# Kernel optimization log

Hardware: AMD Instinct MI355X
Metric: run time of the kernel (lower is better)

## Reference

```python
import jax, jax.numpy as jnp
import numpy as np

N_NODES = 200000
N_EDGES = 600000
IN_DIM = 130   # hidden_dim + 2
HID = 128
BN_EPS = 1e-5


def setup_inputs() -> dict:
    key = jax.random.key(0)
    ks = jax.random.split(key, 12)
    s = 0.05
    inp = {
        'x': jax.random.normal(ks[0], (N_NODES, IN_DIM), dtype=jnp.float32),
        'edge_index': jax.random.randint(ks[1], (2, N_EDGES), 0, N_NODES, dtype=jnp.int32),
        # SAGEConv 1: lin_l (aggregated neighbors, with bias), lin_r (root, no bias)
        'W1_l': jax.random.normal(ks[2], (IN_DIM, HID), dtype=jnp.float32) * s,
        'b1_l': jnp.zeros((HID,), dtype=jnp.float32),
        'W1_r': jax.random.normal(ks[3], (IN_DIM, HID), dtype=jnp.float32) * s,
        # BatchNorm1d(128) params + running stats (eval mode)
        'g1': jnp.ones((HID,), dtype=jnp.float32),
        'be1': jnp.zeros((HID,), dtype=jnp.float32),
        'rm1': jax.random.normal(ks[4], (HID,), dtype=jnp.float32) * 0.01,
        'rv1': jnp.ones((HID,), dtype=jnp.float32),
        # SAGEConv 2
        'W2_l': jax.random.normal(ks[5], (HID, HID), dtype=jnp.float32) * s,
        'b2_l': jnp.zeros((HID,), dtype=jnp.float32),
        'W2_r': jax.random.normal(ks[6], (HID, HID), dtype=jnp.float32) * s,
        'g2': jnp.ones((HID,), dtype=jnp.float32),
        'be2': jnp.zeros((HID,), dtype=jnp.float32),
        'rm2': jax.random.normal(ks[7], (HID,), dtype=jnp.float32) * 0.01,
        'rv2': jnp.ones((HID,), dtype=jnp.float32),
    }
    return inp


def _sage_mean(x, src, dst, W_l, b_l, W_r, n_nodes):
    # PyG SAGEConv (mean aggr): out = lin_l(mean_{j in N(i)} x_j) + lin_r(x_i)
    msg = x[src]                                                 # [E, F] gather
    agg = jax.ops.segment_sum(msg, dst, num_segments=n_nodes)    # [N, F]
    deg = jax.ops.segment_sum(jnp.ones((src.shape[0], 1), x.dtype), dst,
                              num_segments=n_nodes)              # [N, 1]
    mean = agg / jnp.maximum(deg, 1.0)
    return mean @ W_l + b_l + x @ W_r


def _bn_eval(x, g, b, rm, rv):
    return (x - rm) * (g * jax.lax.rsqrt(rv + BN_EPS)) + b


def reference(x, edge_index, W1_l, b1_l, W1_r, g1, be1, rm1, rv1,
              W2_l, b2_l, W2_r, g2, be2, rm2, rv2):
    src, dst = edge_index[0], edge_index[1]
    n = x.shape[0]
    h = _sage_mean(x, src, dst, W1_l, b1_l, W1_r, n)
    h = jax.nn.relu(_bn_eval(h, g1, be1, rm1, rv1))
    # dropout is identity in eval mode
    h = _sage_mean(h, src, dst, W2_l, b2_l, W2_r, n)
    h = jax.nn.relu(_bn_eval(h, g2, be2, rm2, rv2))
    return h
```

## Files before the change

kernel.cpp:

```cpp
#include <hip/hip_runtime.h>

typedef short v8s __attribute__((ext_vector_type(8)));
typedef float v4f __attribute__((ext_vector_type(4)));
typedef unsigned short v4us __attribute__((ext_vector_type(4)));

__device__ __forceinline__ unsigned short f2bf(float x) {
  union { float f; unsigned int u; } c; c.f = x;
  unsigned int u = c.u;
  return (unsigned short)((u + 0x7fffu + ((u >> 16) & 1u)) >> 16);
}
__device__ __forceinline__ float bf2f(unsigned int hi16) {
  union { unsigned int u; float f; } c; c.u = hi16 << 16;
  return c.f;
}
__device__ __forceinline__ ushort2 pk(float2 v) {
  ushort2 p; p.x = f2bf(v.x); p.y = f2bf(v.y); return p;
}

__global__ void bn_fold_k(const float* __restrict__ g1, const float* __restrict__ be1,
                          const float* __restrict__ rm1, const float* __restrict__ rv1,
                          const float* __restrict__ b1,
                          const float* __restrict__ g2, const float* __restrict__ be2,
                          const float* __restrict__ rm2, const float* __restrict__ rv2,
                          const float* __restrict__ b2,
                          float* __restrict__ s1, float* __restrict__ t1,
                          float* __restrict__ s2, float* __restrict__ t2,
                          unsigned short* __restrict__ bufA, int N) {
  int i = threadIdx.x;
  if (i < 128) {
    float sv = g1[i] * rsqrtf(rv1[i] + 1e-5f);
    s1[i] = sv; t1[i] = (b1[i] - rm1[i]) * sv + be1[i];
    float sw = g2[i] * rsqrtf(rv2[i] + 1e-5f);
    s2[i] = sw; t2[i] = (b2[i] - rm2[i]) * sw + be2[i];
  }
  if (i < 64) ((unsigned int*)(bufA + (long)N * 128))[i] = 0u;
}

template<int K, int KC>
__global__ void pack1_k(const float* __restrict__ W, unsigned short* __restrict__ wpk) {
  int i = blockIdx.x * 256 + threadIdx.x;
  if (i >= KC * 4096) return;
  int kk = i & 31, n = (i >> 5) & 127, kc = i >> 12;
  int k = kc * 32 + kk;
  wpk[i] = (k < K) ? f2bf(W[k * 128 + n]) : (unsigned short)0;
}

__global__ void zero_i_k(int* __restrict__ p, int n) {
  int i = blockIdx.x * 256 + threadIdx.x;
  if (i < n) p[i] = 0;
}
__global__ void count_k(const int* __restrict__ dst, int* __restrict__ degi, int E) {
  int i = blockIdx.x * 256 + threadIdx.x;
  if (i < E) atomicAdd(&degi[dst[i]], 1);
}
__global__ __launch_bounds__(256) void scan1_k(const int* __restrict__ degi,
                                               int* __restrict__ rowptr,
                                               int* __restrict__ bsum, int N) {
  __shared__ int sd[256];
  const int t = threadIdx.x;
  const int base = blockIdx.x * 1024 + t * 4;
  int v[4];
#pragma unroll
  for (int j = 0; j < 4; ++j) v[j] = (base + j < N) ? degi[base + j] : 0;
  const int tot = v[0] + v[1] + v[2] + v[3];
  sd[t] = tot;
  __syncthreads();
  for (int off = 1; off < 256; off <<= 1) {
    int o = (t >= off) ? sd[t - off] : 0;
    __syncthreads();
    sd[t] += o;
    __syncthreads();
  }
  int e = sd[t] - tot;
#pragma unroll
  for (int j = 0; j < 4; ++j) {
    if (base + j < N) rowptr[base + j] = e;
    e += v[j];
  }
  if (t == 255) bsum[blockIdx.x] = sd[255];
}
__global__ __launch_bounds__(256) void scan2_k(int* __restrict__ bsum, int nb) {
  __shared__ int sd[256];
  const int t = threadIdx.x;
  const int v = (t < nb) ? bsum[t] : 0;
  sd[t] = v;
  __syncthreads();
  for (int off = 1; off < 256; off <<= 1) {
    int o = (t >= off) ? sd[t - off] : 0;
    __syncthreads();
    sd[t] += o;
    __syncthreads();
  }
  if (t < nb) bsum[t] = sd[t] - v;
}
__global__ void scan3_k(int* __restrict__ rowptr, int* __restrict__ cursor,
                        const int* __restrict__ bsum, int N, int E) {
  int i = blockIdx.x * 256 + threadIdx.x;
  if (i < N) {
    int v = rowptr[i] + bsum[i >> 10];
    rowptr[i] = v;
    cursor[i] = v;
  } else if (i == N) {
    rowptr[N] = E;
  }
}
__global__ void fill_k(const int* __restrict__ src, const int* __restrict__ dst,
                       int* __restrict__ cursor, int* __restrict__ nbr, int E) {
  int i = blockIdx.x * 256 + threadIdx.x;
  if (i < E) {
    int p = atomicAdd(&cursor[dst[i]], 1);
    nbr[p] = src[i];
  }
}

template<int KC, bool SRCF32>
__global__ __launch_bounds__(256) void gemmL_k(const void* __restrict__ Asrc,
                                               const unsigned short* __restrict__ wpk,
                                               unsigned short* __restrict__ O, int N) {
  constexpr int KP = KC * 32;
  constexpr int LDA = KP + 8;
  __shared__ __align__(16) unsigned short a_s[64][LDA];
  const int tid = threadIdx.x;
  const int node0 = blockIdx.x * 64;

  if constexpr (SRCF32) {
    {
      const int zr = tid >> 2, zq = tid & 3;
      v8s z = {0, 0, 0, 0, 0, 0, 0, 0};
      *(v8s*)&a_s[zr][136 + zq * 8] = z;
      if (tid < 192) {
        const int r3 = tid / 3, p3 = tid - 3 * r3;
        *(unsigned int*)&a_s[r3][130 + 2 * p3] = 0u;
      }
    }
    const float* xb = (const float*)Asrc + (long)node0 * 130;
    if (node0 + 64 <= N) {
      float4 v[9];
#pragma unroll
      for (int i = 0; i < 9; ++i) {
        const int g = i * 256 + tid;
        if (g < 2080) v[i] = *(const float4*)(xb + 4 * g);
      }
#pragma unroll
      for (int i = 0; i < 9; ++i) {
        const int g = i * 256 + tid;
        if (g < 2080) {
          const int p0 = 2 * g, p1 = 2 * g + 1;
          const int r0_ = (p0 * 4033) >> 18, r1_ = (p1 * 4033) >> 18;
          const int c0_ = p0 - 65 * r0_, c1_ = p1 - 65 * r1_;
          *(ushort2*)&a_s[r0_][2 * c0_] = pk(make_float2(v[i].x, v[i].y));
          *(ushort2*)&a_s[r1_][2 * c1_] = pk(make_float2(v[i].z, v[i].w));
        }
      }
    } else {
      for (int i = 0; i < 9; ++i) {
        const int g = i * 256 + tid;
        if (g < 2080) {
#pragma unroll
          for (int h = 0; h < 2; ++h) {
            const int p = 2 * g + h;
            const int r = (p * 4033) >> 18;
            const int c = p - 65 * r;
            float2 vv = make_float2(0.f, 0.f);
            if (node0 + r < N)
              vv = *(const float2*)((const float*)Asrc + (long)(node0 + r) * 130 + 2 * c);
            *(ushort2*)&a_s[r][2 * c] = pk(vv);
          }
        }
      }
    }
  } else {
    const unsigned short* hb = (const unsigned short*)Asrc + (long)node0 * 128;
    v8s v[KC];
#pragma unroll
    for (int i = 0; i < KC; ++i) {
      const int u = i * 256 + tid;
      const int r = u >> 4;
      v[i] = (v8s){0, 0, 0, 0, 0, 0, 0, 0};
      if (node0 + r < N) v[i] = *(const v8s*)(hb + 8 * u);
    }
#pragma unroll
    for (int i = 0; i < KC; ++i) {
      const int u = i * 256 + tid;
      *(v8s*)&a_s[u >> 4][(u & 15) * 8] = v[i];
    }
  }
  __syncthreads();

  const int wave = tid >> 6, lane = tid & 63;
  const int quad = lane >> 4, l16 = lane & 15;
  v4f acc[4][2];
#pragma unroll
  for (int mt = 0; mt < 4; ++mt)
#pragma unroll
    for (int nt = 0; nt < 2; ++nt) acc[mt][nt] = (v4f){0.f, 0.f, 0.f, 0.f};

  const unsigned short* wb = wpk + (wave * 32 + l16) * 32 + quad * 8;
#pragma unroll
  for (int kc = 0; kc < KC; ++kc) {
    v8s wf[2];
#pragma unroll
    for (int nt = 0; nt < 2; ++nt)
      wf[nt] = *(const v8s*)(wb + kc * 4096 + nt * 512);
#pragma unroll
    for (int mt = 0; mt < 4; ++mt) {
      v8s nf = *(const v8s*)(&a_s[mt * 16 + l16][kc * 32 + quad * 8]);
#pragma unroll
      for (int nt = 0; nt < 2; ++nt)
        acc[mt][nt] = __builtin_amdgcn_mfma_f32_16x16x32_bf16(wf[nt], nf, acc[mt][nt], 0, 0, 0);
    }
  }

#pragma unroll
  for (int mt = 0; mt < 4; ++mt) {
    const int rw = node0 + mt * 16 + l16;
    if (rw < N) {
#pragma unroll
      for (int nt = 0; nt < 2; ++nt) {
        const int oc = wave * 32 + nt * 16 + quad * 4;
        v4us v;
        v[0] = f2bf(acc[mt][nt][0]);
        v[1] = f2bf(acc[mt][nt][1]);
        v[2] = f2bf(acc[mt][nt][2]);
        v[3] = f2bf(acc[mt][nt][3]);
        *(v4us*)(O + (long)rw * 128 + oc) = v;
      }
    }
  }
}

template<int KC, bool SRCF32, bool OUTF32>
__global__ __launch_bounds__(256) void spmmR_k(const unsigned short* __restrict__ gsrc,
                                               const void* __restrict__ rsrc,
                                               const unsigned short* __restrict__ wpkr,
                                               const int* __restrict__ rowptr,
                                               const int* __restrict__ nbr,
                                               const float* __restrict__ sc,
                                               const float* __restrict__ tc,
                                               void* __restrict__ out, int N, int E) {
  constexpr int LXS = SRCF32 ? 168 : 136;
  __shared__ __align__(16) unsigned short xls[16][LXS];
  __shared__ __align__(16) float rls[16][132];
  const int tid = threadIdx.x;
  const int lane = tid & 63;
  const int wu = __builtin_amdgcn_readfirstlane(tid >> 6);
  const int quad = lane >> 4, l16 = lane & 15;
  const int nb0 = blockIdx.x * 16;

  if constexpr (SRCF32) {
    {
      if (tid < 64) {
        v8s z = {0, 0, 0, 0, 0, 0, 0, 0};
        *(v8s*)&xls[tid >> 2][136 + (tid & 3) * 8] = z;
      }
      if (tid < 48) {
        const int r3 = tid / 3, p3 = tid - 3 * r3;
        *(unsigned int*)&xls[r3][130 + 2 * p3] = 0u;
      }
    }
    const float* xb = (const float*)rsrc + (long)nb0 * 130;
    if (nb0 + 16 <= N) {
      float4 v[3];
#pragma unroll
      for (int i = 0; i < 3; ++i) {
        const int g = i * 256 + tid;
        if (g < 520) v[i] = *(const float4*)(xb + 4 * g);
      }
#pragma unroll
      for (int i = 0; i < 3; ++i) {
        const int g = i * 256 + tid;
        if (g < 520) {
          const int p0 = 2 * g, p1 = 2 * g + 1;
          const int r0_ = (p0 * 4033) >> 18, r1_ = (p1 * 4033) >> 18;
          const int c0_ = p0 - 65 * r0_, c1_ = p1 - 65 * r1_;
          *(ushort2*)&xls[r0_][2 * c0_] = pk(make_float2(v[i].x, v[i].y));
          *(ushort2*)&xls[r1_][2 * c1_] = pk(make_float2(v[i].z, v[i].w));
        }
      }
    } else {
      for (int i = 0; i < 3; ++i) {
        const int g = i * 256 + tid;
        if (g < 520) {
#pragma unroll
          for (int h = 0; h < 2; ++h) {
            const int p = 2 * g + h;
            const int r = (p * 4033) >> 18;
            const int c = p - 65 * r;
            float2 vv = make_float2(0.f, 0.f);
            if (nb0 + r < N)
              vv = *(const float2*)((const float*)rsrc + (long)(nb0 + r) * 130 + 2 * c);
            *(ushort2*)&xls[r][2 * c] = pk(vv);
          }
        }
      }
    }
  } else {
    const unsigned short* hb = (const unsigned short*)rsrc + (long)nb0 * 128;
    const int r = tid >> 4, c = (tid & 15) * 8;
    v8s v = {0, 0, 0, 0, 0, 0, 0, 0};
    if (nb0 + r < N) v = *(const v8s*)(hb + (long)r * 128 + c);
    *(v8s*)&xls[r][c] = v;
  }

  const int nb = nb0 + wu * 4;
  int r0[4], d[4];
#pragma unroll
  for (int r = 0; r < 4; ++r) {
    const int i0 = min(nb + r, N);
    const int i1 = min(nb + r + 1, N);
    r0[r] = rowptr[i0];
    const int r1 = rowptr[i1];
    d[r] = (nb + r < N) ? (r1 - r0[r]) : 0;
  }
  const int dm = max(max(d[0], d[1]), max(d[2], d[3]));
  float2 a[4];
#pragma unroll
  for (int r = 0; r < 4; ++r) a[r] = make_float2(0.f, 0.f);

  __syncthreads();

  {
    v4f racc[2];
    racc[0] = (v4f){0.f, 0.f, 0.f, 0.f};
    racc[1] = (v4f){0.f, 0.f, 0.f, 0.f};
    const unsigned short* wb = wpkr + (wu * 32 + l16) * 32 + quad * 8;
#pragma unroll
    for (int kc = 0; kc < KC; ++kc) {
      v8s nf = *(const v8s*)&xls[l16][kc * 32 + quad * 8];
#pragma unroll
      for (int nt = 0; nt < 2; ++nt) {
        v8s wf = *(const v8s*)(wb + kc * 4096 + nt * 512);
        racc[nt] = __builtin_amdgcn_mfma_f32_16x16x32_bf16(wf, nf, racc[nt], 0, 0, 0);
      }
    }
#pragma unroll
    for (int nt = 0; nt < 2; ++nt)
      *(v4f*)&rls[l16][wu * 32 + nt * 16 + quad * 4] = racc[nt];
  }

  const int lofs = lane << 1;
  for (int e0 = 0; e0 < dm; e0 += 8) {
    unsigned int u[4][8];
#pragma unroll
    for (int j = 0; j < 8; ++j)
#pragma unroll
      for (int r = 0; r < 4; ++r) {
        const int e = e0 + j;
        const int nv = nbr[min(r0[r] + e, E - 1)];
        const int idx = (e < d[r]) ? nv : N;
        u[r][j] = *(const unsigned int*)(gsrc + ((long)idx << 7) + lofs);
      }
#pragma unroll
    for (int r = 0; r < 4; ++r)
#pragma unroll
      for (int j = 0; j < 8; ++j) {
        a[r].x += bf2f(u[r][j] & 0xffffu);
        a[r].y += bf2f(u[r][j] >> 16);
      }
  }

  __syncthreads();

  const float2 sv = *(const float2*)(sc + 2 * lane);
  const float2 tv = *(const float2*)(tc + 2 * lane);
#pragma unroll
  for (int r = 0; r < 4; ++r) {
    if (nb + r < N) {
      const float inv = 1.0f / fmaxf((float)d[r], 1.0f);
      const float2 rt = *(const float2*)&rls[wu * 4 + r][2 * lane];
      float yx = a[r].x * inv + rt.x;
      float yy = a[r].y * inv + rt.y;
      yx = fmaxf(yx * sv.x + tv.x, 0.f);
      yy = fmaxf(yy * sv.y + tv.y, 0.f);
      if (OUTF32) {
        *(float2*)((float*)out + (long)(nb + r) * 128 + 2 * lane) = make_float2(yx, yy);
      } else {
        *(ushort2*)((unsigned short*)out + (long)(nb + r) * 128 + 2 * lane) =
            pk(make_float2(yx, yy));
      }
    }
  }
}

extern "C" void kernel_launch(void* const* d_in, const int* in_sizes, int n_in,
                              void* d_out, int out_size, void* d_ws, size_t ws_size,
                              hipStream_t stream) {
  const float* x   = (const float*)d_in[0];
  const int*   ei  = (const int*)d_in[1];
  const float* W1l = (const float*)d_in[2];
  const float* b1  = (const float*)d_in[3];
  const float* W1r = (const float*)d_in[4];
  const float* g1  = (const float*)d_in[5];
  const float* be1 = (const float*)d_in[6];
  const float* rm1 = (const float*)d_in[7];
  const float* rv1 = (const float*)d_in[8];
  const float* W2l = (const float*)d_in[9];
  const float* b2  = (const float*)d_in[10];
  const float* W2r = (const float*)d_in[11];
  const float* g2  = (const float*)d_in[12];
  const float* be2 = (const float*)d_in[13];
  const float* rm2 = (const float*)d_in[14];
  const float* rv2 = (const float*)d_in[15];

  const int E = in_sizes[1] / 2;
  const int N = in_sizes[0] / 130;
  const int* src = ei;
  const int* dst = ei + E;

  unsigned short* bufA = (unsigned short*)d_ws;
  unsigned short* bufB = bufA + (size_t)(N + 1) * 128;
  unsigned short* wp1l = bufB + (size_t)(N + 1) * 128;
  unsigned short* wp1r = wp1l + 5 * 4096;
  unsigned short* wp2l = wp1r + 5 * 4096;
  unsigned short* wp2r = wp2l + 4 * 4096;
  float* s1 = (float*)(wp2r + 4 * 4096);
  float* t1 = s1 + 128;
  float* s2 = t1 + 128;
  float* t2 = s2 + 128;
  int* degi   = (int*)(t2 + 128);
  int* rowptr = degi + N;
  int* bsum   = rowptr + N + 1;
  int* nbr    = bsum + 256;

  hipLaunchKernelGGL(bn_fold_k, dim3(1), dim3(128), 0, stream,
                     g1, be1, rm1, rv1, b1, g2, be2, rm2, rv2, b2,
                     s1, t1, s2, t2, bufA, N);
  hipLaunchKernelGGL((pack1_k<130, 5>), dim3(80), dim3(256), 0, stream, W1l, wp1l);
  hipLaunchKernelGGL((pack1_k<130, 5>), dim3(80), dim3(256), 0, stream, W1r, wp1r);
  hipLaunchKernelGGL((pack1_k<128, 4>), dim3(64), dim3(256), 0, stream, W2l, wp2l);
  hipLaunchKernelGGL((pack1_k<128, 4>), dim3(64), dim3(256), 0, stream, W2r, wp2r);

  hipLaunchKernelGGL(zero_i_k, dim3((N + 255) / 256), dim3(256), 0, stream, degi, N);
  hipLaunchKernelGGL(count_k, dim3((E + 255) / 256), dim3(256), 0, stream, dst, degi, E);
  const int nb = (N + 1023) / 1024;
  hipLaunchKernelGGL(scan1_k, dim3(nb), dim3(256), 0, stream, degi, rowptr, bsum, N);
  hipLaunchKernelGGL(scan2_k, dim3(1), dim3(256), 0, stream, bsum, nb);
  hipLaunchKernelGGL(scan3_k, dim3((N + 256) / 256), dim3(256), 0, stream,
                     rowptr, degi, bsum, N, E);
  hipLaunchKernelGGL(fill_k, dim3((E + 255) / 256), dim3(256), 0, stream,
                     src, dst, degi, nbr, E);

  const int ngb = (N + 63) / 64;
  const int nsb = (N + 15) / 16;

  hipLaunchKernelGGL((gemmL_k<5, true>), dim3(ngb), dim3(256), 0, stream,
                     (const void*)x, wp1l, bufA, N);
  hipLaunchKernelGGL((spmmR_k<5, true, false>), dim3(nsb), dim3(256), 0, stream,
                     bufA, (const void*)x, wp1r, rowptr, nbr, s1, t1, (void*)bufB, N, E);
  hipLaunchKernelGGL((gemmL_k<4, false>), dim3(ngb), dim3(256), 0, stream,
                     (const void*)bufB, wp2l, bufA, N);
  hipLaunchKernelGGL((spmmR_k<4, false, true>), dim3(nsb), dim3(256), 0, stream,
                     bufA, (const void*)bufB, wp2r, rowptr, nbr, s2, t2, d_out, N, E);
}
```

Baseline: 435.9 us.

## Fuse layer-2 transforms into layer-1 SpMM epilogue, drop separate layer-2 GEMM

```diff
diff --git a/kernel.cpp b/kernel.cpp
--- a/kernel.cpp
+++ b/kernel.cpp
@@ -25,7 +25,8 @@
                           const float* __restrict__ b2,
                           float* __restrict__ s1, float* __restrict__ t1,
                           float* __restrict__ s2, float* __restrict__ t2,
-                          unsigned short* __restrict__ bufA, int N) {
+                          unsigned short* __restrict__ bufA,
+                          unsigned short* __restrict__ bufB, int N) {
   int i = threadIdx.x;
   if (i < 128) {
     float sv = g1[i] * rsqrtf(rv1[i] + 1e-5f);
@@ -33,7 +34,10 @@
     float sw = g2[i] * rsqrtf(rv2[i] + 1e-5f);
     s2[i] = sw; t2[i] = (b2[i] - rm2[i]) * sw + be2[i];
   }
-  if (i < 64) ((unsigned int*)(bufA + (long)N * 128))[i] = 0u;
+  if (i < 64) {
+    ((unsigned int*)(bufA + (long)N * 128))[i] = 0u;
+    ((unsigned int*)(bufB + (long)N * 128))[i] = 0u;
+  }
 }
 
 template<int K, int KC>
@@ -113,8 +117,8 @@
   }
 }
 
-template<int KC, bool SRCF32>
-__global__ __launch_bounds__(256) void gemmL_k(const void* __restrict__ Asrc,
+template<int KC>
+__global__ __launch_bounds__(256) void gemmL_k(const float* __restrict__ Asrc,
                                                const unsigned short* __restrict__ wpk,
                                                unsigned short* __restrict__ O, int N) {
   constexpr int KP = KC * 32;
@@ -123,66 +127,49 @@
   const int tid = threadIdx.x;
   const int node0 = blockIdx.x * 64;
 
-  if constexpr (SRCF32) {
-    {
-      const int zr = tid >> 2, zq = tid & 3;
-      v8s z = {0, 0, 0, 0, 0, 0, 0, 0};
-      *(v8s*)&a_s[zr][136 + zq * 8] = z;
-      if (tid < 192) {
-        const int r3 = tid / 3, p3 = tid - 3 * r3;
-        *(unsigned int*)&a_s[r3][130 + 2 * p3] = 0u;
-      }
-    }
-    const float* xb = (const float*)Asrc + (long)node0 * 130;
-    if (node0 + 64 <= N) {
-      float4 v[9];
-#pragma unroll
-      for (int i = 0; i < 9; ++i) {
-        const int g = i * 256 + tid;
-        if (g < 2080) v[i] = *(const float4*)(xb + 4 * g);
-      }
-#pragma unroll
-      for (int i = 0; i < 9; ++i) {
-        const int g = i * 256 + tid;
-        if (g < 2080) {
-          const int p0 = 2 * g, p1 = 2 * g + 1;
-          const int r0_ = (p0 * 4033) >> 18, r1_ = (p1 * 4033) >> 18;
-          const int c0_ = p0 - 65 * r0_, c1_ = p1 - 65 * r1_;
-          *(ushort2*)&a_s[r0_][2 * c0_] = pk(make_float2(v[i].x, v[i].y));
-          *(ushort2*)&a_s[r1_][2 * c1_] = pk(make_float2(v[i].z, v[i].w));
+  {
+    const int zr = tid >> 2, zq = tid & 3;
+    v8s z = {0, 0, 0, 0, 0, 0, 0, 0};
+    *(v8s*)&a_s[zr][136 + zq * 8] = z;
+    if (tid < 192) {
+      const int r3 = tid / 3, p3 = tid - 3 * r3;
+      *(unsigned int*)&a_s[r3][130 + 2 * p3] = 0u;
+    }
+  }
+  const float* xb = Asrc + (long)node0 * 130;
+  if (node0 + 64 <= N) {
+    float4 v[9];
+#pragma unroll
+    for (int i = 0; i < 9; ++i) {
+      const int g = i * 256 + tid;
+      if (g < 2080) v[i] = *(const float4*)(xb + 4 * g);
+    }
+#pragma unroll
+    for (int i = 0; i < 9; ++i) {
+      const int g = i * 256 + tid;
+      if (g < 2080) {
+        const int p0 = 2 * g, p1 = 2 * g + 1;
+        const int r0_ = (p0 * 4033) >> 18, r1_ = (p1 * 4033) >> 18;
+        const int c0_ = p0 - 65 * r0_, c1_ = p1 - 65 * r1_;
+        *(ushort2*)&a_s[r0_][2 * c0_] = pk(make_float2(v[i].x, v[i].y));
+        *(ushort2*)&a_s[r1_][2 * c1_] = pk(make_float2(v[i].z, v[i].w));
+      }
+    }
+  } else {
+    for (int i = 0; i < 9; ++i) {
+      const int g = i * 256 + tid;
+      if (g < 2080) {
+#pragma unroll
+        for (int h = 0; h < 2; ++h) {
+          const int p = 2 * g + h;
+          const int r = (p * 4033) >> 18;
+          const int c = p - 65 * r;
+          float2 vv = make_float2(0.f, 0.f);
+          if (node0 + r < N)
+            vv = *(const float2*)(Asrc + (long)(node0 + r) * 130 + 2 * c);
+          *(ushort2*)&a_s[r][2 * c] = pk(vv);
         }
       }
-    } else {
-      for (int i = 0; i < 9; ++i) {
-        const int g = i * 256 + tid;
-        if (g < 2080) {
-#pragma unroll
-          for (int h = 0; h < 2; ++h) {
-            const int p = 2 * g + h;
-            const int r = (p * 4033) >> 18;
-            const int c = p - 65 * r;
-            float2 vv = make_float2(0.f, 0.f);
-            if (node0 + r < N)
-              vv = *(const float2*)((const float*)Asrc + (long)(node0 + r) * 130 + 2 * c);
-            *(ushort2*)&a_s[r][2 * c] = pk(vv);
-          }
-        }
-      }
-    }
-  } else {
-    const unsigned short* hb = (const unsigned short*)Asrc + (long)node0 * 128;
-    v8s v[KC];
-#pragma unroll
-    for (int i = 0; i < KC; ++i) {
-      const int u = i * 256 + tid;
-      const int r = u >> 4;
-      v[i] = (v8s){0, 0, 0, 0, 0, 0, 0, 0};
-      if (node0 + r < N) v[i] = *(const v8s*)(hb + 8 * u);
-    }
-#pragma unroll
-    for (int i = 0; i < KC; ++i) {
-      const int u = i * 256 + tid;
-      *(v8s*)&a_s[u >> 4][(u & 15) * 8] = v[i];
     }
   }
   __syncthreads();
@@ -229,77 +216,73 @@
   }
 }
 
-template<int KC, bool SRCF32, bool OUTF32>
-__global__ __launch_bounds__(256) void spmmR_k(const unsigned short* __restrict__ gsrc,
-                                               const void* __restrict__ rsrc,
+template<int KC>
+__global__ __launch_bounds__(256) void spmmF_k(const unsigned short* __restrict__ gsrc,
+                                               const float* __restrict__ xsrc,
                                                const unsigned short* __restrict__ wpkr,
+                                               const unsigned short* __restrict__ w2l,
+                                               const unsigned short* __restrict__ w2r,
                                                const int* __restrict__ rowptr,
                                                const int* __restrict__ nbr,
                                                const float* __restrict__ sc,
                                                const float* __restrict__ tc,
-                                               void* __restrict__ out, int N, int E) {
-  constexpr int LXS = SRCF32 ? 168 : 136;
-  __shared__ __align__(16) unsigned short xls[16][LXS];
+                                               unsigned short* __restrict__ P2l,
+                                               unsigned short* __restrict__ P2r,
+                                               int N, int E) {
+  __shared__ __align__(16) unsigned short xls[16][168];
   __shared__ __align__(16) float rls[16][132];
+  __shared__ __align__(16) unsigned short h1s[16][136];
   const int tid = threadIdx.x;
   const int lane = tid & 63;
   const int wu = __builtin_amdgcn_readfirstlane(tid >> 6);
   const int quad = lane >> 4, l16 = lane & 15;
   const int nb0 = blockIdx.x * 16;
 
-  if constexpr (SRCF32) {
-    {
-      if (tid < 64) {
-        v8s z = {0, 0, 0, 0, 0, 0, 0, 0};
-        *(v8s*)&xls[tid >> 2][136 + (tid & 3) * 8] = z;
-      }
-      if (tid < 48) {
-        const int r3 = tid / 3, p3 = tid - 3 * r3;
-        *(unsigned int*)&xls[r3][130 + 2 * p3] = 0u;
-      }
-    }
-    const float* xb = (const float*)rsrc + (long)nb0 * 130;
-    if (nb0 + 16 <= N) {
-      float4 v[3];
-#pragma unroll
-      for (int i = 0; i < 3; ++i) {
-        const int g = i * 256 + tid;
-        if (g < 520) v[i] = *(const float4*)(xb + 4 * g);
-      }
-#pragma unroll
-      for (int i = 0; i < 3; ++i) {
-        const int g = i * 256 + tid;
-        if (g < 520) {
-          const int p0 = 2 * g, p1 = 2 * g + 1;
-          const int r0_ = (p0 * 4033) >> 18, r1_ = (p1 * 4033) >> 18;
-          const int c0_ = p0 - 65 * r0_, c1_ = p1 - 65 * r1_;
-          *(ushort2*)&xls[r0_][2 * c0_] = pk(make_float2(v[i].x, v[i].y));
-          *(ushort2*)&xls[r1_][2 * c1_] = pk(make_float2(v[i].z, v[i].w));
+  {
+    if (tid < 64) {
+      v8s z = {0, 0, 0, 0, 0, 0, 0, 0};
+      *(v8s*)&xls[tid >> 2][136 + (tid & 3) * 8] = z;
+    }
+    if (tid < 48) {
+      const int r3 = tid / 3, p3 = tid - 3 * r3;
+      *(unsigned int*)&xls[r3][130 + 2 * p3] = 0u;
+    }
+  }
+  const float* xb = xsrc + (long)nb0 * 130;
+  if (nb0 + 16 <= N) {
+    float4 v[3];
+#pragma unroll
+    for (int i = 0; i < 3; ++i) {
+      const int g = i * 256 + tid;
+      if (g < 520) v[i] = *(const float4*)(xb + 4 * g);
+    }
+#pragma unroll
+    for (int i = 0; i < 3; ++i) {
+      const int g = i * 256 + tid;
+      if (g < 520) {
+        const int p0 = 2 * g, p1 = 2 * g + 1;
+        const int r0_ = (p0 * 4033) >> 18, r1_ = (p1 * 4033) >> 18;
+        const int c0_ = p0 - 65 * r0_, c1_ = p1 - 65 * r1_;
+        *(ushort2*)&xls[r0_][2 * c0_] = pk(make_float2(v[i].x, v[i].y));
+        *(ushort2*)&xls[r1_][2 * c1_] = pk(make_float2(v[i].z, v[i].w));
+      }
+    }
+  } else {
+    for (int i = 0; i < 3; ++i) {
+      const int g = i * 256 + tid;
+      if (g < 520) {
+#pragma unroll
+        for (int h = 0; h < 2; ++h) {
+          const int p = 2 * g + h;
+          const int r = (p * 4033) >> 18;
+          const int c = p - 65 * r;
+          float2 vv = make_float2(0.f, 0.f);
+          if (nb0 + r < N)
+            vv = *(const float2*)(xsrc + (long)(nb0 + r) * 130 + 2 * c);
+          *(ushort2*)&xls[r][2 * c] = pk(vv);
         }
       }
-    } else {
-      for (int i = 0; i < 3; ++i) {
-        const int g = i * 256 + tid;
-        if (g < 520) {
-#pragma unroll
-          for (int h = 0; h < 2; ++h) {
-            const int p = 2 * g + h;
-            const int r = (p * 4033) >> 18;
-            const int c = p - 65 * r;
-            float2 vv = make_float2(0.f, 0.f);
-            if (nb0 + r < N)
-              vv = *(const float2*)((const float*)rsrc + (long)(nb0 + r) * 130 + 2 * c);
-            *(ushort2*)&xls[r][2 * c] = pk(vv);
-          }
-        }
-      }
-    }
-  } else {
-    const unsigned short* hb = (const unsigned short*)rsrc + (long)nb0 * 128;
-    const int r = tid >> 4, c = (tid & 15) * 8;
-    v8s v = {0, 0, 0, 0, 0, 0, 0, 0};
-    if (nb0 + r < N) v = *(const v8s*)(hb + (long)r * 128 + c);
-    *(v8s*)&xls[r][c] = v;
+    }
   }
 
   const int nb = nb0 + wu * 4;
@@ -361,23 +344,111 @@
 
   __syncthreads();
 
+  {
+    const float2 sv = *(const float2*)(sc + 2 * lane);
+    const float2 tv = *(const float2*)(tc + 2 * lane);
+#pragma unroll
+    for (int r = 0; r < 4; ++r) {
+      const float inv = 1.0f / fmaxf((float)d[r], 1.0f);
+      const float2 rt = *(const float2*)&rls[wu * 4 + r][2 * lane];
+      float yx = fmaxf((a[r].x * inv + rt.x) * sv.x + tv.x, 0.f);
+      float yy = fmaxf((a[r].y * inv + rt.y) * sv.y + tv.y, 0.f);
+      *(ushort2*)&h1s[wu * 4 + r][2 * lane] = pk(make_float2(yx, yy));
+    }
+  }
+
+  __syncthreads();
+
+  {
+    unsigned short* ob = (wu < 2) ? P2l : P2r;
+    const unsigned short* w2 = (wu < 2) ? w2l : w2r;
+    const int cb = (wu & 1) * 64;
+    v4f acc[4];
+#pragma unroll
+    for (int nt = 0; nt < 4; ++nt) acc[nt] = (v4f){0.f, 0.f, 0.f, 0.f};
+    const unsigned short* wb2 = w2 + (cb + l16) * 32 + quad * 8;
+#pragma unroll
+    for (int kc = 0; kc < 4; ++kc) {
+      v8s nf = *(const v8s*)&h1s[l16][kc * 32 + quad * 8];
+#pragma unroll
+      for (int nt = 0; nt < 4; ++nt) {
+        v8s wf = *(const v8s*)(wb2 + kc * 4096 + nt * 512);
+        acc[nt] = __builtin_amdgcn_mfma_f32_16x16x32_bf16(wf, nf, acc[nt], 0, 0, 0);
+      }
+    }
+    const int rw = nb0 + l16;
+    if (rw < N) {
+#pragma unroll
+      for (int nt = 0; nt < 4; ++nt) {
+        const int oc = cb + nt * 16 + quad * 4;
+        v4us v;
+        v[0] = f2bf(acc[nt][0]);
+        v[1] = f2bf(acc[nt][1]);
+        v[2] = f2bf(acc[nt][2]);
+        v[3] = f2bf(acc[nt][3]);
+        *(v4us*)(ob + (long)rw * 128 + oc) = v;
+      }
+    }
+  }
+}
+
+__global__ __launch_bounds__(256) void spmmL_k(const unsigned short* __restrict__ gsrc,
+                                               const unsigned short* __restrict__ rsrc,
+                                               const int* __restrict__ rowptr,
+                                               const int* __restrict__ nbr,
+                                               const float* __restrict__ sc,
+                                               const float* __restrict__ tc,
+                                               float* __restrict__ out, int N, int E) {
+  const int tid = threadIdx.x;
+  const int lane = tid & 63;
+  const int wu = __builtin_amdgcn_readfirstlane(tid >> 6);
+  const int nb = blockIdx.x * 16 + wu * 4;
+
+  int r0[4], d[4];
+#pragma unroll
+  for (int r = 0; r < 4; ++r) {
+    const int i0 = min(nb + r, N);
+    const int i1 = min(nb + r + 1, N);
+    r0[r] = rowptr[i0];
+    const int r1 = rowptr[i1];
+    d[r] = (nb + r < N) ? (r1 - r0[r]) : 0;
+  }
+  const int dm = max(max(d[0], d[1]), max(d[2], d[3]));
+  float2 a[4];
+#pragma unroll
+  for (int r = 0; r < 4; ++r) a[r] = make_float2(0.f, 0.f);
+
+  const int lofs = lane << 1;
+  for (int e0 = 0; e0 < dm; e0 += 8) {
+    unsigned int u[4][8];
+#pragma unroll
+    for (int j = 0; j < 8; ++j)
+#pragma unroll
+      for (int r = 0; r < 4; ++r) {
+        const int e = e0 + j;
+        const int nv = nbr[min(r0[r] + e, E - 1)];
+        const int idx = (e < d[r]) ? nv : N;
+        u[r][j] = *(const unsigned int*)(gsrc + ((long)idx << 7) + lofs);
+      }
+#pragma unroll
+    for (int r = 0; r < 4; ++r)
+#pragma unroll
+      for (int j = 0; j < 8; ++j) {
+        a[r].x += bf2f(u[r][j] & 0xffffu);
+        a[r].y += bf2f(u[r][j] >> 16);
+      }
+  }
+
   const float2 sv = *(const float2*)(sc + 2 * lane);
   const float2 tv = *(const float2*)(tc + 2 * lane);
 #pragma unroll
   for (int r = 0; r < 4; ++r) {
     if (nb + r < N) {
       const float inv = 1.0f / fmaxf((float)d[r], 1.0f);
-      const float2 rt = *(const float2*)&rls[wu * 4 + r][2 * lane];
-      float yx = a[r].x * inv + rt.x;
-      float yy = a[r].y * inv + rt.y;
-      yx = fmaxf(yx * sv.x + tv.x, 0.f);
-      yy = fmaxf(yy * sv.y + tv.y, 0.f);
-      if (OUTF32) {
-        *(float2*)((float*)out + (long)(nb + r) * 128 + 2 * lane) = make_float2(yx, yy);
-      } else {
-        *(ushort2*)((unsigned short*)out + (long)(nb + r) * 128 + 2 * lane) =
-            pk(make_float2(yx, yy));
-      }
+      const unsigned int ur = *(const unsigned int*)(rsrc + ((long)(nb + r) << 7) + lofs);
+      float yx = fmaxf((a[r].x * inv + bf2f(ur & 0xffffu)) * sv.x + tv.x, 0.f);
+      float yy = fmaxf((a[r].y * inv + bf2f(ur >> 16)) * sv.y + tv.y, 0.f);
+      *(float2*)(out + (long)(nb + r) * 128 + 2 * lane) = make_float2(yx, yy);
     }
   }
 }
@@ -409,7 +480,8 @@
 
   unsigned short* bufA = (unsigned short*)d_ws;
   unsigned short* bufB = bufA + (size_t)(N + 1) * 128;
-  unsigned short* wp1l = bufB + (size_t)(N + 1) * 128;
+  unsigned short* bufC = bufB + (size_t)(N + 1) * 128;
+  unsigned short* wp1l = bufC + (size_t)N * 128;
   unsigned short* wp1r = wp1l + 5 * 4096;
   unsigned short* wp2l = wp1r + 5 * 4096;
   unsigned short* wp2r = wp2l + 4 * 4096;
@@ -424,7 +496,7 @@
 
   hipLaunchKernelGGL(bn_fold_k, dim3(1), dim3(128), 0, stream,
                      g1, be1, rm1, rv1, b1, g2, be2, rm2, rv2, b2,
-                     s1, t1, s2, t2, bufA, N);
+                     s1, t1, s2, t2, bufA, bufB, N);
   hipLaunchKernelGGL((pack1_k<130, 5>), dim3(80), dim3(256), 0, stream, W1l, wp1l);
   hipLaunchKernelGGL((pack1_k<130, 5>), dim3(80), dim3(256), 0, stream, W1r, wp1r);
   hipLaunchKernelGGL((pack1_k<128, 4>), dim3(64), dim3(256), 0, stream, W2l, wp2l);
@@ -443,12 +515,10 @@
   const int ngb = (N + 63) / 64;
   const int nsb = (N + 15) / 16;
 
-  hipLaunchKernelGGL((gemmL_k<5, true>), dim3(ngb), dim3(256), 0, stream,
-                     (const void*)x, wp1l, bufA, N);
-  hipLaunchKernelGGL((spmmR_k<5, true, false>), dim3(nsb), dim3(256), 0, stream,
-                     bufA, (const void*)x, wp1r, rowptr, nbr, s1, t1, (void*)bufB, N, E);
-  hipLaunchKernelGGL((gemmL_k<4, false>), dim3(ngb), dim3(256), 0, stream,
-                     (const void*)bufB, wp2l, bufA, N);
-  hipLaunchKernelGGL((spmmR_k<4, false, true>), dim3(nsb), dim3(256), 0, stream,
-                     bufA, (const void*)bufB, wp2r, rowptr, nbr, s2, t2, d_out, N, E);
-}
+  hipLaunchKernelGGL((gemmL_k<5>), dim3(ngb), dim3(256), 0, stream, x, wp1l, bufA, N);
+  hipLaunchKernelGGL((spmmF_k<5>), dim3(nsb), dim3(256), 0, stream,
+                     bufA, x, wp1r, wp2l, wp2r, rowptr, nbr, s1, t1,
+                     bufB, bufC, N, E);
+  hipLaunchKernelGGL(spmmL_k, dim3(nsb), dim3(256), 0, stream,
+                     bufB, bufC, rowptr, nbr, s2, t2, (float*)d_out, N, E);
+}
```

Result: slower. 455.8 us (+4.6%).
